# Optimization experiments

Measured on AMD Instinct MI355X. Metric: run time of the kernel, lower is better.

The kernel has to match this reference:

```python
import jax, jax.numpy as jnp
import numpy as np

B, S, L, D, M = 32, 256, 64, 100, 20  # batch, n_sentences, max_sentence_len, embed_dim, n_memories


def setup_inputs() -> dict:
    key = jax.random.key(0)
    ks = jax.random.split(key, 6)
    batch = jax.random.normal(ks[0], (B, S, L, D), dtype=jnp.float32)
    enc_mult = jnp.ones((L, D), dtype=jnp.float32)  # input_encoder_multiplier (init to ones)
    keys = 0.1 * jax.random.normal(ks[1], (M, D), dtype=jnp.float32)
    U = 0.1 * jax.random.normal(ks[2], (D, D), dtype=jnp.float32)  # nn.Linear weight [out,in]
    V = 0.1 * jax.random.normal(ks[3], (D, D), dtype=jnp.float32)
    W = 0.1 * jax.random.normal(ks[4], (D, D), dtype=jnp.float32)
    prelu_a = jnp.ones((), dtype=jnp.float32)  # PReLU(init=1), single shared parameter
    return {"batch": batch, "enc_mult": enc_mult, "keys": keys, "U": U, "V": V, "W": W, "prelu_a": prelu_a}


def reference(batch, enc_mult, keys, U, V, W, prelu_a):
    # Encode: elementwise multiply by learned positional multiplier, sum over words -> [B, S, D]
    enc = (batch * enc_mult).sum(axis=2)

    def prelu(x):
        return jnp.where(x >= 0, x, prelu_a * x)

    # keys @ V.T is step-invariant
    keysV = jnp.einsum('md,ed->me', keys, V)  # [M, D]

    def step(mem, s):  # mem: [B, M, D], s: [B, D]
        memory_gate = jnp.einsum('bd,bmd->bm', s, mem)          # [B, M]
        key_gate = jnp.einsum('bd,md->bm', s, keys)              # [B, M]
        gate = jax.nn.sigmoid(memory_gate + key_gate)            # [B, M]
        cand = prelu(
            jnp.einsum('bmd,ed->bme', mem, U)                    # U(memories)
            + keysV[None, :, :]                                  # V(keys)
            + jnp.einsum('bd,ed->be', s, W)[:, None, :]          # W(sentence), broadcast over M
        )
        mem = mem + cand * gate[:, :, None]
        mem = mem / jnp.linalg.norm(mem, axis=2, keepdims=True)  # L2 normalize each memory slot
        return mem, None

    mem0 = jnp.broadcast_to(keys[None, :, :], (B, M, D))  # memories init = keys repeated per batch
    mem_final, _ = jax.lax.scan(step, mem0, jnp.swapaxes(enc, 0, 1))  # scan over sentences
    return mem_final
```

## Files before the change

### kernel.cpp

```cpp
#include <hip/hip_runtime.h>


typedef float v2f __attribute__((ext_vector_type(2)));

__global__ __launch_bounds__(256) void encode_k(
    const float* __restrict__ batch,
    const float* __restrict__ encm,
    float* __restrict__ enc)
{
    const int tid = blockIdx.x * 256 + threadIdx.x;
    const int r = tid / 25;
    const int c = tid % 25;
    const float4* b4 = (const float4*)batch + (size_t)r * 1600 + c;
    const float4* e4 = (const float4*)encm + c;
    float4 acc = {0.f, 0.f, 0.f, 0.f};
    #pragma unroll 8
    for (int l = 0; l < 64; ++l) {
        float4 x  = b4[l * 25];
        float4 mu = e4[l * 25];
        acc.x += x.x * mu.x;
        acc.y += x.y * mu.y;
        acc.z += x.z * mu.z;
        acc.w += x.w * mu.w;
    }
    ((float4*)enc)[(size_t)r * 25 + c] = acc;
}

__global__ __launch_bounds__(128) void project_k(
    const float* __restrict__ enc,
    const float* __restrict__ W,
    float* __restrict__ sWp)
{
    const int t = threadIdx.x;
    if (t >= 100) return;
    const int row0 = blockIdx.x * 4;
    const float4* w4 = (const float4*)(W + t * 100);
    const float4* e0 = (const float4*)(enc + (size_t)row0 * 100);
    const float4* e1 = e0 + 25;
    const float4* e2 = e0 + 50;
    const float4* e3 = e0 + 75;
    float a0 = 0.f, a1 = 0.f, a2 = 0.f, a3 = 0.f;
    #pragma unroll
    for (int k = 0; k < 25; ++k) {
        float4 w = w4[k];
        float4 s0 = e0[k], s1 = e1[k], s2 = e2[k], s3 = e3[k];
        a0 += w.x * s0.x + w.y * s0.y + w.z * s0.z + w.w * s0.w;
        a1 += w.x * s1.x + w.y * s1.y + w.z * s1.z + w.w * s1.w;
        a2 += w.x * s2.x + w.y * s2.y + w.z * s2.z + w.w * s2.w;
        a3 += w.x * s3.x + w.y * s3.y + w.z * s3.z + w.w * s3.w;
    }
    sWp[(size_t)row0 * 100 + t]       = a0;
    sWp[(size_t)(row0 + 1) * 100 + t] = a1;
    sWp[(size_t)(row0 + 2) * 100 + t] = a2;
    sWp[(size_t)(row0 + 3) * 100 + t] = a3;
}

template <int CTRL>
__device__ __forceinline__ float dpp_add_f(float x) {
    int s = __builtin_amdgcn_update_dpp(0, __float_as_int(x), CTRL, 0xF, 0xF, true);
    return x + __int_as_float(s);
}
__device__ __forceinline__ float lane63(float x) {
    return __int_as_float(__builtin_amdgcn_readlane(__float_as_int(x), 63));
}

__global__ __launch_bounds__(64, 1) void entnet_scan(
    const float* __restrict__ enc,
    const float* __restrict__ sWp,
    const float* __restrict__ keys,
    const float* __restrict__ U,
    const float* __restrict__ V,
    const float* __restrict__ paPtr,
    float* __restrict__ out)
{
    __shared__ float memL[100];
    const int lane = threadIdx.x;
    const int b = blockIdx.x / 20;
    const int m = blockIdx.x % 20;
    const bool hi = (lane < 36);
    const float h = hi ? 1.f : 0.f;
    const int e0 = lane;
    const int e1 = hi ? (64 + lane) : 99;
    const float pa = paPtr[0];

    v2f Upk[100];
    {
        const float4* u0 = (const float4*)(U + e0 * 100);
        const float4* u1 = (const float4*)(U + e1 * 100);
        #pragma unroll
        for (int k = 0; k < 25; ++k) {
            float4 a = u0[k], c = u1[k];
            Upk[4 * k + 0] = (v2f){a.x, c.x};
            Upk[4 * k + 1] = (v2f){a.y, c.y};
            Upk[4 * k + 2] = (v2f){a.z, c.z};
            Upk[4 * k + 3] = (v2f){a.w, c.w};
        }
    }
    v2f kV = (v2f){0.f, 0.f};
    {
        const float4* km = (const float4*)(keys + m * 100);
        const float4* v0 = (const float4*)(V + e0 * 100);
        const float4* v1 = (const float4*)(V + e1 * 100);
        #pragma unroll
        for (int k = 0; k < 25; ++k) {
            float4 kk = km[k], a = v0[k], c = v1[k];
            kV.x += a.x * kk.x + a.y * kk.y + a.z * kk.z + a.w * kk.w;
            kV.y += c.x * kk.x + c.y * kk.y + c.z * kk.z + c.w * kk.w;
        }
    }
    const float k0 = keys[m * 100 + e0];
    const float k1 = h * keys[m * 100 + e1];
    float mem0 = k0, mem1 = k1;
    memL[e0] = mem0;
    if (hi) memL[e1] = mem1;
    __asm__ __volatile__("" ::: "memory");

    const float* encRow = enc + (size_t)b * 25600;
    const float* sWRow  = sWp + (size_t)b * 25600;

    float sv0 = encRow[e0], sv1 = encRow[e1];
    float sw0 = sWRow[e0],  sw1 = sWRow[e1];

    for (int step = 0; step < 256; ++step) {
        const int nxt = (step < 255 ? step + 1 : 255) * 100;
        const float nsv0 = encRow[nxt + e0], nsv1 = encRow[nxt + e1];
        const float nsw0 = sWRow[nxt + e0], nsw1 = sWRow[nxt + e1];

        v2f acc = (v2f){0.f, 0.f};
        const float4* m4 = (const float4*)memL;
        #pragma unroll
        for (int k = 0; k < 25; ++k) {
            float4 v = m4[k];
            acc += Upk[4 * k + 0] * v.x;
            acc += Upk[4 * k + 1] * v.y;
            acc += Upk[4 * k + 2] * v.z;
            acc += Upk[4 * k + 3] * v.w;
        }
        float c0 = acc.x + kV.x + sw0;
        float c1 = acc.y + kV.y + sw1;
        c0 = (c0 >= 0.f) ? c0 : pa * c0;
        c1 = (c1 >= 0.f) ? c1 : pa * c1;

        float p0 = mem0 * mem0 + mem1 * mem1;
        float p1 = sv0 * mem0 + sv1 * mem1;
        float p2 = sv0 * k0 + sv1 * k1;
        float p3 = mem0 * c0 + mem1 * c1;
        float p4 = c0 * c0 + h * c1 * c1;

        #define RND(C) p0 = dpp_add_f<C>(p0); p1 = dpp_add_f<C>(p1); \
                       p2 = dpp_add_f<C>(p2); p3 = dpp_add_f<C>(p3); p4 = dpp_add_f<C>(p4);
        RND(0x111) RND(0x112) RND(0x114) RND(0x118) RND(0x142) RND(0x143)
        #undef RND
        const float s0 = lane63(p0);
        const float s1 = lane63(p1);
        const float s2 = lane63(p2);
        const float s3 = lane63(p3);
        const float s4 = lane63(p4);

        const float g  = 1.f / (1.f + __expf(-(s1 + s2)));
        const float n2 = s0 + 2.f * g * s3 + g * g * s4;
        const float rn = rsqrtf(n2);
        mem0 = (mem0 + g * c0) * rn;
        mem1 = h * (mem1 + g * c1) * rn;
        memL[e0] = mem0;
        if (hi) memL[e1] = mem1;
        __asm__ __volatile__("" ::: "memory");

        sv0 = nsv0; sv1 = nsv1; sw0 = nsw0; sw1 = nsw1;
    }
    float* orow = out + (size_t)(b * 20 + m) * 100;
    orow[e0] = mem0;
    if (hi) orow[e1] = mem1;
}

extern "C" void kernel_launch(void* const* d_in, const int* in_sizes, int n_in,
                              void* d_out, int out_size, void* d_ws, size_t ws_size,
                              hipStream_t stream) {
    const float* batch = (const float*)d_in[0];
    const float* encm  = (const float*)d_in[1];
    const float* keys  = (const float*)d_in[2];
    const float* U     = (const float*)d_in[3];
    const float* V     = (const float*)d_in[4];
    const float* W     = (const float*)d_in[5];
    const float* pa    = (const float*)d_in[6];
    float* out = (float*)d_out;

    float* enc = (float*)d_ws;
    float* sWp = enc + 819200;

    encode_k<<<800, 256, 0, stream>>>(batch, encm, enc);
    project_k<<<2048, 128, 0, stream>>>(enc, W, sWp);
    entnet_scan<<<640, 64, 0, stream>>>(enc, sWp, keys, U, V, pa, out);
}
```

Measured before the change: 519.5 us.

## Defer normalization, precompute key gate, restage encode through LDS

The scan now stores unnormalized memory and folds the reciprocal norm into the next step's matvec and gate. This removes the mem·mem reduction and moves the normalization off the LDS store path, so three cross-lane reductions remain per step instead of five. The key-gate dot product s·keys is computed up front in the projection kernel and read per step. The matvec is split into five independent accumulators to shorten the dependency chain. The encode kernel is rewritten to use 64-thread blocks that preload the multiplier into registers and reduce over words through LDS, which adds barriers and large shared-memory use per block.

Result: slower. 554.9 us (+6.8%).

```diff
diff --git a/kernel.cpp b/kernel.cpp
--- a/kernel.cpp
+++ b/kernel.cpp
@@ -3,38 +3,71 @@
 
 typedef float v2f __attribute__((ext_vector_type(2)));
 
-__global__ __launch_bounds__(256) void encode_k(
+__global__ __launch_bounds__(64) void encode_k(
     const float* __restrict__ batch,
     const float* __restrict__ encm,
     float* __restrict__ enc)
 {
-    const int tid = blockIdx.x * 256 + threadIdx.x;
-    const int r = tid / 25;
-    const int c = tid % 25;
-    const float4* b4 = (const float4*)batch + (size_t)r * 1600 + c;
-    const float4* e4 = (const float4*)encm + c;
-    float4 acc = {0.f, 0.f, 0.f, 0.f};
-    #pragma unroll 8
-    for (int l = 0; l < 64; ++l) {
-        float4 x  = b4[l * 25];
-        float4 mu = e4[l * 25];
-        acc.x += x.x * mu.x;
-        acc.y += x.y * mu.y;
-        acc.z += x.z * mu.z;
-        acc.w += x.w * mu.w;
-    }
-    ((float4*)enc)[(size_t)r * 25 + c] = acc;
+    __shared__ float4 stage[1600];
+    __shared__ float4 part[50];
+    const int lane = threadIdx.x;
+    float4 MU[25];
+    const float4* e4 = (const float4*)encm;
+    #pragma unroll
+    for (int i = 0; i < 25; ++i) MU[i] = e4[i * 64 + lane];
+    const int q = (lane >= 25) ? 1 : 0;
+    const int c = lane - 25 * q;
+    const bool red = (lane < 50);
+
+    for (int r8 = 0; r8 < 8; ++r8) {
+        const int row = blockIdx.x * 8 + r8;
+        const float4* rb = (const float4*)batch + (size_t)row * 1600;
+        #pragma unroll
+        for (int i = 0; i < 25; ++i) {
+            float4 x = rb[i * 64 + lane];
+            float4 mu = MU[i];
+            float4 p;
+            p.x = x.x * mu.x; p.y = x.y * mu.y; p.z = x.z * mu.z; p.w = x.w * mu.w;
+            stage[i * 64 + lane] = p;
+        }
+        __syncthreads();
+        float4 a0 = {0.f,0.f,0.f,0.f}, a1 = {0.f,0.f,0.f,0.f};
+        if (red) {
+            const int l0 = 32 * q;
+            #pragma unroll
+            for (int k = 0; k < 32; k += 2) {
+                float4 u = stage[(l0 + k) * 25 + c];
+                float4 v = stage[(l0 + k + 1) * 25 + c];
+                a0.x += u.x; a0.y += u.y; a0.z += u.z; a0.w += u.w;
+                a1.x += v.x; a1.y += v.y; a1.z += v.z; a1.w += v.w;
+            }
+            float4 s;
+            s.x = a0.x + a1.x; s.y = a0.y + a1.y; s.z = a0.z + a1.z; s.w = a0.w + a1.w;
+            part[lane] = s;
+        }
+        __syncthreads();
+        if (lane < 25) {
+            float4 s = part[lane], t2 = part[lane + 25];
+            float4 o;
+            o.x = s.x + t2.x; o.y = s.y + t2.y; o.z = s.z + t2.z; o.w = s.w + t2.w;
+            ((float4*)enc)[(size_t)row * 25 + lane] = o;
+        }
+        __syncthreads();
+    }
 }
 
 __global__ __launch_bounds__(128) void project_k(
     const float* __restrict__ enc,
     const float* __restrict__ W,
-    float* __restrict__ sWp)
+    const float* __restrict__ keys,
+    float* __restrict__ sWp,
+    float* __restrict__ kg)
 {
     const int t = threadIdx.x;
-    if (t >= 100) return;
+    if (t >= 120) return;
+    const float* wrow = (t < 100) ? (W + t * 100) : (keys + (t - 100) * 100);
     const int row0 = blockIdx.x * 4;
-    const float4* w4 = (const float4*)(W + t * 100);
+    const float4* w4 = (const float4*)wrow;
     const float4* e0 = (const float4*)(enc + (size_t)row0 * 100);
     const float4* e1 = e0 + 25;
     const float4* e2 = e0 + 50;
@@ -49,10 +82,18 @@
         a2 += w.x * s2.x + w.y * s2.y + w.z * s2.z + w.w * s2.w;
         a3 += w.x * s3.x + w.y * s3.y + w.z * s3.z + w.w * s3.w;
     }
-    sWp[(size_t)row0 * 100 + t]       = a0;
-    sWp[(size_t)(row0 + 1) * 100 + t] = a1;
-    sWp[(size_t)(row0 + 2) * 100 + t] = a2;
-    sWp[(size_t)(row0 + 3) * 100 + t] = a3;
+    if (t < 100) {
+        sWp[(size_t)row0 * 100 + t]       = a0;
+        sWp[(size_t)(row0 + 1) * 100 + t] = a1;
+        sWp[(size_t)(row0 + 2) * 100 + t] = a2;
+        sWp[(size_t)(row0 + 3) * 100 + t] = a3;
+    } else {
+        const int m = t - 100;
+        kg[(size_t)row0 * 20 + m]       = a0;
+        kg[(size_t)(row0 + 1) * 20 + m] = a1;
+        kg[(size_t)(row0 + 2) * 20 + m] = a2;
+        kg[(size_t)(row0 + 3) * 20 + m] = a3;
+    }
 }
 
 template <int CTRL>
@@ -67,13 +108,15 @@
 __global__ __launch_bounds__(64, 1) void entnet_scan(
     const float* __restrict__ enc,
     const float* __restrict__ sWp,
+    const float* __restrict__ kg,
     const float* __restrict__ keys,
     const float* __restrict__ U,
     const float* __restrict__ V,
     const float* __restrict__ paPtr,
     float* __restrict__ out)
 {
-    __shared__ float memL[100];
+    __shared__ float4 mem4[32];
+    float* memF = (float*)mem4;
     const int lane = threadIdx.x;
     const int b = blockIdx.x / 20;
     const int m = blockIdx.x % 20;
@@ -96,7 +139,7 @@
             Upk[4 * k + 3] = (v2f){a.w, c.w};
         }
     }
-    v2f kV = (v2f){0.f, 0.f};
+    float kv0 = 0.f, kv1 = 0.f;
     {
         const float4* km = (const float4*)(keys + m * 100);
         const float4* v0 = (const float4*)(V + e0 * 100);
@@ -104,73 +147,84 @@
         #pragma unroll
         for (int k = 0; k < 25; ++k) {
             float4 kk = km[k], a = v0[k], c = v1[k];
-            kV.x += a.x * kk.x + a.y * kk.y + a.z * kk.z + a.w * kk.w;
-            kV.y += c.x * kk.x + c.y * kk.y + c.z * kk.z + c.w * kk.w;
+            kv0 += a.x * kk.x + a.y * kk.y + a.z * kk.z + a.w * kk.w;
+            kv1 += c.x * kk.x + c.y * kk.y + c.z * kk.z + c.w * kk.w;
         }
     }
     const float k0 = keys[m * 100 + e0];
     const float k1 = h * keys[m * 100 + e1];
-    float mem0 = k0, mem1 = k1;
-    memL[e0] = mem0;
-    if (hi) memL[e1] = mem1;
+    float nm0 = k0, nm1 = k1;
+    memF[lane] = nm0;
+    memF[64 + lane] = nm1;
     __asm__ __volatile__("" ::: "memory");
+
+    float nq = k0 * k0 + k1 * k1;
+    nq = dpp_add_f<0x111>(nq); nq = dpp_add_f<0x112>(nq); nq = dpp_add_f<0x114>(nq);
+    nq = dpp_add_f<0x118>(nq); nq = dpp_add_f<0x142>(nq); nq = dpp_add_f<0x143>(nq);
+    float nsq = lane63(nq);
+    float rn = 1.f;
 
     const float* encRow = enc + (size_t)b * 25600;
     const float* sWRow  = sWp + (size_t)b * 25600;
+    const float* kgRow  = kg + (size_t)b * 5120 + m;
 
     float sv0 = encRow[e0], sv1 = encRow[e1];
     float sw0 = sWRow[e0],  sw1 = sWRow[e1];
+    float kgc = kgRow[0];
 
     for (int step = 0; step < 256; ++step) {
-        const int nxt = (step < 255 ? step + 1 : 255) * 100;
-        const float nsv0 = encRow[nxt + e0], nsv1 = encRow[nxt + e1];
-        const float nsw0 = sWRow[nxt + e0], nsw1 = sWRow[nxt + e1];
-
-        v2f acc = (v2f){0.f, 0.f};
-        const float4* m4 = (const float4*)memL;
-        #pragma unroll
-        for (int k = 0; k < 25; ++k) {
-            float4 v = m4[k];
-            acc += Upk[4 * k + 0] * v.x;
-            acc += Upk[4 * k + 1] * v.y;
-            acc += Upk[4 * k + 2] * v.z;
-            acc += Upk[4 * k + 3] * v.w;
-        }
-        float c0 = acc.x + kV.x + sw0;
-        float c1 = acc.y + kV.y + sw1;
-        c0 = (c0 >= 0.f) ? c0 : pa * c0;
-        c1 = (c1 >= 0.f) ? c1 : pa * c1;
-
-        float p0 = mem0 * mem0 + mem1 * mem1;
-        float p1 = sv0 * mem0 + sv1 * mem1;
-        float p2 = sv0 * k0 + sv1 * k1;
-        float p3 = mem0 * c0 + mem1 * c1;
-        float p4 = c0 * c0 + h * c1 * c1;
-
-        #define RND(C) p0 = dpp_add_f<C>(p0); p1 = dpp_add_f<C>(p1); \
-                       p2 = dpp_add_f<C>(p2); p3 = dpp_add_f<C>(p3); p4 = dpp_add_f<C>(p4);
-        RND(0x111) RND(0x112) RND(0x114) RND(0x118) RND(0x142) RND(0x143)
-        #undef RND
-        const float s0 = lane63(p0);
-        const float s1 = lane63(p1);
-        const float s2 = lane63(p2);
-        const float s3 = lane63(p3);
-        const float s4 = lane63(p4);
-
-        const float g  = 1.f / (1.f + __expf(-(s1 + s2)));
-        const float n2 = s0 + 2.f * g * s3 + g * g * s4;
-        const float rn = rsqrtf(n2);
-        mem0 = (mem0 + g * c0) * rn;
-        mem1 = h * (mem1 + g * c1) * rn;
-        memL[e0] = mem0;
-        if (hi) memL[e1] = mem1;
+        const int nxt = (step < 255 ? step + 1 : 255);
+        const float nsv0 = encRow[nxt * 100 + e0], nsv1 = encRow[nxt * 100 + e1];
+        const float nsw0 = sWRow[nxt * 100 + e0], nsw1 = sWRow[nxt * 100 + e1];
+        const float nkg  = kgRow[nxt * 20];
+
+        v2f A0 = {0.f,0.f}, A1 = {0.f,0.f}, A2 = {0.f,0.f}, A3 = {0.f,0.f}, A4 = {0.f,0.f};
+        #pragma unroll
+        for (int k = 0; k < 25; k += 5) {
+            float4 v0 = mem4[k],     v1 = mem4[k + 1], v2 = mem4[k + 2];
+            float4 v3 = mem4[k + 3], v4 = mem4[k + 4];
+            A0 += Upk[4*k+0]*v0.x;      A0 += Upk[4*k+1]*v0.y;      A0 += Upk[4*k+2]*v0.z;      A0 += Upk[4*k+3]*v0.w;
+            A1 += Upk[4*(k+1)+0]*v1.x;  A1 += Upk[4*(k+1)+1]*v1.y;  A1 += Upk[4*(k+1)+2]*v1.z;  A1 += Upk[4*(k+1)+3]*v1.w;
+            A2 += Upk[4*(k+2)+0]*v2.x;  A2 += Upk[4*(k+2)+1]*v2.y;  A2 += Upk[4*(k+2)+2]*v2.z;  A2 += Upk[4*(k+2)+3]*v2.w;
+            A3 += Upk[4*(k+3)+0]*v3.x;  A3 += Upk[4*(k+3)+1]*v3.y;  A3 += Upk[4*(k+3)+2]*v3.z;  A3 += Upk[4*(k+3)+3]*v3.w;
+            A4 += Upk[4*(k+4)+0]*v4.x;  A4 += Upk[4*(k+4)+1]*v4.y;  A4 += Upk[4*(k+4)+2]*v4.z;  A4 += Upk[4*(k+4)+3]*v4.w;
+        }
+        v2f acc = ((A0 + A1) + (A2 + A3)) + A4;
+
+        float x0 = rn * acc.x + kv0 + sw0;
+        float x1 = rn * acc.y + kv1 + sw1;
+        float c0 = (x0 >= 0.f) ? x0 : pa * x0;
+        float c1 = (x1 >= 0.f) ? x1 : pa * x1;
+        c1 *= h;
+
+        float q1 = sv0 * nm0 + sv1 * nm1;
+        float q3 = nm0 * c0 + nm1 * c1;
+        float p4 = c0 * c0 + c1 * c1;
+        #define RND3(C) q1 = dpp_add_f<C>(q1); q3 = dpp_add_f<C>(q3); p4 = dpp_add_f<C>(p4);
+        RND3(0x111) RND3(0x112) RND3(0x114) RND3(0x118) RND3(0x142) RND3(0x143)
+        #undef RND3
+        const float Q1 = lane63(q1);
+        const float Q3 = lane63(q3);
+        const float P4 = lane63(p4);
+
+        const float g = 1.f / (1.f + __expf(-(rn * Q1 + kgc)));
+
+        nm0 = rn * nm0 + g * c0;
+        nm1 = rn * nm1 + g * c1;
+        memF[lane] = nm0;
+        memF[64 + lane] = nm1;
         __asm__ __volatile__("" ::: "memory");
 
-        sv0 = nsv0; sv1 = nsv1; sw0 = nsw0; sw1 = nsw1;
+        const float grn = g * rn;
+        const float n2 = nsq + 2.f * grn * Q3 + g * g * P4;
+        rn = rsqrtf(n2);
+        nsq = 1.f;
+
+        sv0 = nsv0; sv1 = nsv1; sw0 = nsw0; sw1 = nsw1; kgc = nkg;
     }
     float* orow = out + (size_t)(b * 20 + m) * 100;
-    orow[e0] = mem0;
-    if (hi) orow[e1] = mem1;
+    orow[e0] = nm0 * rn;
+    if (hi) orow[e1] = nm1 * rn;
 }
 
 extern "C" void kernel_launch(void* const* d_in, const int* in_sizes, int n_in,
@@ -187,8 +241,9 @@
 
     float* enc = (float*)d_ws;
     float* sWp = enc + 819200;
-
-    encode_k<<<800, 256, 0, stream>>>(batch, encm, enc);
-    project_k<<<2048, 128, 0, stream>>>(enc, W, sWp);
-    entnet_scan<<<640, 64, 0, stream>>>(enc, sWp, keys, U, V, pa, out);
-}
+    float* kgb = sWp + 819200;
+
+    encode_k<<<1024, 64, 0, stream>>>(batch, encm, enc);
+    project_k<<<2048, 128, 0, stream>>>(enc, W, keys, sWp, kgb);
+    entnet_scan<<<640, 64, 0, stream>>>(enc, sWp, kgb, keys, U, V, pa, out);
+}
```
